# Kernel tuning notes

Measured on AMD Instinct MI355X. Metric: run time of the kernel, lower is better.

Reference implementation:

```python
import jax, jax.numpy as jnp
import numpy as np

B, N, C, H, KH = 4, 4096, 1024, 16, 5
HD = C // H  # head dim = 64


def setup_inputs() -> dict:
    key = jax.random.key(0)
    ks = jax.random.split(key, 4)
    return {
        "x": jax.random.normal(ks[0], (B, N, C), jnp.float32),
        "qkv_w": jax.random.normal(ks[1], (3 * C, C), jnp.float32) * 0.02,
        "qkv_b": jnp.zeros((3 * C,), jnp.float32),
        "proj_w": jax.random.normal(ks[2], (C, C), jnp.float32) * 0.02,
        "proj_b": jnp.zeros((C,), jnp.float32),
        "pos_enc": jnp.zeros((1, C), jnp.float32),  # torch init: zeros
        "dwc_w": jax.random.normal(ks[3], (HD, 1, KH, KH), jnp.float32) * 0.05,
        "dwc_b": jnp.zeros((HD,), jnp.float32),
        "num_heads": H,
    }


def reference(x, qkv_w, qkv_b, proj_w, proj_b, pos_enc, dwc_w, dwc_b, num_heads):
    b, n, c = x.shape
    h = num_heads
    hd = c // h
    kh = dwc_w.shape[2]

    qkv = x @ qkv_w.T + qkv_b                     # (b, n, 3c)
    q, k, v = jnp.split(qkv, 3, axis=-1)          # each (b, n, c)
    k = k + pos_enc[:, :c]                        # broadcast (1, c)
    q = jax.nn.relu(q)
    k = jax.nn.relu(k)

    def to_heads(t):  # (b, n, c) -> (b*h, n, hd)
        return t.reshape(b, n, h, hd).transpose(0, 2, 1, 3).reshape(b * h, n, hd)

    q, k, v = to_heads(q), to_heads(k), to_heads(v)

    # linear attention in fp32 (inputs already fp32)
    z = 1.0 / (jnp.einsum('bic,bc->bi', q, k.sum(axis=1)) + 1e-6)   # (bh, n)
    kv = jnp.einsum('bjc,bjd->bcd', k, v)                           # (bh, hd, hd)
    out = jnp.einsum('bic,bcd->bid', q, kv) * z[:, :, None]         # (bh, n, hd)

    # depthwise 2D conv on v viewed as (bh, hd, n, 1), kernel (hd,1,kh,kh), pad kh//2
    fm = v.transpose(0, 2, 1)[..., None]                            # (bh, hd, n, 1)
    pad = kh // 2
    fm = jax.lax.conv_general_dilated(
        fm, dwc_w, window_strides=(1, 1),
        padding=((pad, pad), (pad, pad)),
        dimension_numbers=('NCHW', 'OIHW', 'NCHW'),
        feature_group_count=hd,
    ) + dwc_b[None, :, None, None]
    out = out + fm[..., 0].transpose(0, 2, 1)                       # (bh, n, hd)

    out = out.reshape(b, h, n, hd).transpose(0, 2, 1, 3).reshape(b, n, c)
    return out @ proj_w.T + proj_b
```

## Files before the change

### kernel.cpp

```cpp
#include <hip/hip_runtime.h>


#define BB   4
#define NN   4096
#define CDIM 1024
#define NH   16
#define HDIM 64
#define BH   64

typedef __attribute__((ext_vector_type(8))) short short8;
typedef __attribute__((ext_vector_type(4))) float f32x4;
typedef unsigned short u16;

__device__ __forceinline__ float b2f(short s) {
    union { unsigned u; float f; } c;
    c.u = ((unsigned)(unsigned short)s) << 16;
    return c.f;
}
__device__ __forceinline__ u16 f2b(float f) {
    unsigned u = __float_as_uint(f);
    return (u16)((u + 0x7fffu + ((u >> 16) & 1u)) >> 16);
}
__device__ __forceinline__ void gload16(const void* g, void* l) {
    __builtin_amdgcn_global_load_lds((const __attribute__((address_space(1))) void*)g,
                                     (__attribute__((address_space(3))) void*)l, 16, 0, 0);
}

__global__ __launch_bounds__(256) void k_fill_diag(float* __restrict__ out, int n, float val)
{
    int i = blockIdx.x * 256 + threadIdx.x;
    if (i < n) out[i] = val;
}

__global__ __launch_bounds__(256) void k_f32_to_bf16(const float* __restrict__ in,
                                                     u16* __restrict__ out, int n4)
{
    int i = blockIdx.x * 256 + threadIdx.x;
    if (i < n4) {
        float4 v = reinterpret_cast<const float4*>(in)[i];
        ushort4 o;
        o.x = f2b(v.x); o.y = f2b(v.y); o.z = f2b(v.z); o.w = f2b(v.w);
        reinterpret_cast<ushort4*>(out)[i] = o;
    }
}


#define GEMM_PROLOGUE_AND_LOOP(EXTRA_BCOLS)                                              \
    const int t = threadIdx.x;                                                           \
    const int l = t & 63, w = t >> 6;                                                    \
    const int wr = w >> 2, wc = w & 3;                                                   \
    const int qa = ((l & 3) ^ ((l >> 3) & 3)) * 8;                                       \
    const int srow = t >> 2;                                                             \
    const u16* gA = A  + (size_t)(brow + srow) * 1024 + qa;                              \
    const u16* gB = Bw + (size_t)(bcol + srow) * 1024 + qa;                              \
    const int fr = l & 15;                                                               \
    const int phys8 = ((l >> 4) ^ ((l >> 1) & 3)) * 8;                                   \
    const int arow0 = wr * 128 + fr;                                                     \
    const int bfr0  = wc * 64 + fr;                                                      \
    f32x4 acc[8][4];                                                                     \
    _Pragma("unroll")                                                                    \
    for (int m = 0; m < 8; ++m)                                                          \
        _Pragma("unroll")                                                                \
        for (int n = 0; n < 4; ++n) acc[m][n] = (f32x4){0.f, 0.f, 0.f, 0.f};             \
                                              \
    auto STAGE = [&](int buf, int kt) {                                                  \
        const int kof = kt * 32;                                                         \
        char* lb = (char*)lds + buf * 32768 + w * 1024;                                  \
        gload16(gA + kof,          lb);                                                  \
        gload16(gA + 131072 + kof, lb + 8192);                                           \
        gload16(gB + kof,          lb + 16384);                                          \
        gload16(gB + 131072 + kof, lb + 24576);                                          \
    };                                                                                   \
    STAGE(0, 0);                                                                         \
    STAGE(1, 1);                                                                         \
    asm volatile("s_waitcnt vmcnt(4)" ::: "memory");                                     \
    __builtin_amdgcn_sched_barrier(0);                                                   \
    __builtin_amdgcn_s_barrier();                                                        \
    __builtin_amdgcn_sched_barrier(0);                                                   \
    for (int kt = 0; kt < 32; ++kt) {                                                    \
        const int cur = kt & 1;                                                          \
        const int ab = cur * 16384;                                                      \
        short8 af[8], bf[4];                                                             \
        _Pragma("unroll")                                                                \
        for (int n = 0; n < 4; ++n)                                                      \
            bf[n] = *reinterpret_cast<const short8*>(                                    \
                        &lds[ab + 8192 + (bfr0 + n * 16) * 32 + phys8]);                 \
        _Pragma("unroll")                                                                \
        for (int m = 0; m < 8; ++m)                                                      \
            af[m] = *reinterpret_cast<const short8*>(                                    \
                        &lds[ab + (arow0 + m * 16) * 32 + phys8]);                       \
        asm volatile("s_waitcnt lgkmcnt(0)" ::: "memory");                               \
        __builtin_amdgcn_sched_barrier(0);                                               \
        __builtin_amdgcn_s_barrier();               \
        __builtin_amdgcn_sched_barrier(0);                                               \
        if (kt + 2 < 32) STAGE(cur, kt + 2);                                             \
        __builtin_amdgcn_s_setprio(1);                                                   \
        _Pragma("unroll")                                                                \
        for (int m = 0; m < 8; ++m)                                                      \
            _Pragma("unroll")                                                            \
            for (int n = 0; n < 4; ++n)                                                  \
                acc[m][n] = __builtin_amdgcn_mfma_f32_16x16x32_bf16(                     \
                                af[m], bf[n], acc[m][n], 0, 0, 0);                       \
        __builtin_amdgcn_s_setprio(0);                                                   \
        if (kt + 2 < 32) { asm volatile("s_waitcnt vmcnt(4)" ::: "memory"); }            \
        else             { asm volatile("s_waitcnt vmcnt(0)" ::: "memory"); }            \
        __builtin_amdgcn_sched_barrier(0);                                               \
        __builtin_amdgcn_s_barrier();                 \
        __builtin_amdgcn_sched_barrier(0);                                               \
    }

__global__ __launch_bounds__(512, 2) void k_gemm1_256(
    const u16* __restrict__ A,
    const u16* __restrict__ Bw,
    const float* __restrict__ bias, const float* __restrict__ pos_enc,
    u16* __restrict__ q, u16* __restrict__ kk_, u16* __restrict__ v)
{
    __shared__ u16 lds[32768];
    const int lid = blockIdx.y * 12 + blockIdx.x;
    const int swz = (lid & 7) * 96 + (lid >> 3);
    const int bcol = (swz % 12) * 256;
    const int brow = (swz / 12) * 256;

    GEMM_PROLOGUE_AND_LOOP()

    const int part = bcol >> 10;
    u16* dst = (part == 0) ? q : (part == 1) ? kk_ : v;
    const int col_base = bcol + wc * 64 + fr;
    const int row_base = brow + wr * 128 + (l >> 4) * 4;
    #pragma unroll
    for (int n = 0; n < 4; ++n) {
        const int gc = col_base + n * 16;
        const int c  = gc & 1023;
        float bv = bias[gc];
        if (part == 1) bv += pos_enc[c];
        const int h = c >> 6, d = c & 63;
        #pragma unroll
        for (int m = 0; m < 8; ++m)
            #pragma unroll
            for (int j = 0; j < 4; ++j) {
                const int gr = row_base + m * 16 + j;
                const int b_ = gr >> 12, i_ = gr & 4095;
                float val = acc[m][n][j] + bv;
                if (part != 2) val = fmaxf(val, 0.f);
                dst[(size_t)((b_ * NH + h) * NN + i_) * HDIM + d] = f2b(val);
            }
    }
}

__global__ __launch_bounds__(512, 2) void k_gemm2_256(
    const u16* __restrict__ A,
    const u16* __restrict__ Bw,
    const float* __restrict__ bias, float* __restrict__ out)
{
    __shared__ u16 lds[32768];
    const int lid = blockIdx.y * 4 + blockIdx.x;
    const int swz = (lid & 7) * 32 + (lid >> 3);
    const int bcol = (swz % 4) * 256;
    const int brow = (swz / 4) * 256;

    GEMM_PROLOGUE_AND_LOOP()

    const int col_base = bcol + wc * 64 + fr;
    const int row_base = brow + wr * 128 + (l >> 4) * 4;
    #pragma unroll
    for (int n = 0; n < 4; ++n) {
        const int gc = col_base + n * 16;
        const float bv = bias[gc];
        #pragma unroll
        for (int m = 0; m < 8; ++m)
            #pragma unroll
            for (int j = 0; j < 4; ++j) {
                const int gr = row_base + m * 16 + j;
                out[(size_t)gr * CDIM + gc] = acc[m][n][j] + bv;
            }
    }
}

__global__ __launch_bounds__(256) void k_kv_partial(
    const u16* __restrict__ k, const u16* __restrict__ v,
    float* __restrict__ part_kv, float* __restrict__ part_ks)
{
    __shared__ float ks[32 * 64];
    __shared__ float vs[32 * 64];
    const int bh = blockIdx.x;
    const int chunk = blockIdx.y;
    const int t = threadIdx.x;
    const int cg = t >> 4;
    const int dg = t & 15;
    const int lr = t >> 3;
    const int lc = (t & 7) * 8;
    const size_t base = (size_t)bh * NN * HDIM + (size_t)chunk * 1024 * HDIM;
    float acc[4][4] = {};
    float ksac[4] = {};
    for (int j0 = 0; j0 < 1024; j0 += 32) {
        short8 kr = *reinterpret_cast<const short8*>(&k[base + (size_t)(j0 + lr) * 64 + lc]);
        short8 vr = *reinterpret_cast<const short8*>(&v[base + (size_t)(j0 + lr) * 64 + lc]);
        __syncthreads();
        #pragma unroll
        for (int j = 0; j < 8; ++j) {
            ks[lr * 64 + lc + j] = b2f(kr[j]);
            vs[lr * 64 + lc + j] = b2f(vr[j]);
        }
        __syncthreads();
        #pragma unroll
        for (int j = 0; j < 32; ++j) {
            float4 k4 = *reinterpret_cast<const float4*>(&ks[j * 64 + cg * 4]);
            float4 v4 = *reinterpret_cast<const float4*>(&vs[j * 64 + dg * 4]);
            const float* kp = reinterpret_cast<const float*>(&k4);
            const float* vp = reinterpret_cast<const float*>(&v4);
            #pragma unroll
            for (int ii = 0; ii < 4; ++ii) {
                ksac[ii] += kp[ii];
                #pragma unroll
                for (int jj = 0; jj < 4; ++jj)
                    acc[ii][jj] += kp[ii] * vp[jj];
            }
        }
    }
    const int pb = (chunk * BH + bh);
    #pragma unroll
    for (int ii = 0; ii < 4; ++ii) {
        #pragma unroll
        for (int jj = 0; jj < 4; ++jj)
            part_kv[pb * 4096 + (cg * 4 + ii) * 64 + dg * 4 + jj] = acc[ii][jj];
        if (dg == 0) part_ks[pb * 64 + cg * 4 + ii] = ksac[ii];
    }
}

__global__ __launch_bounds__(256) void k_kv_reduce_t(
    const float* __restrict__ part_kv, const float* __restrict__ part_ks,
    u16* __restrict__ kvt)
{
    const int bh = blockIdx.x;
    const int t = threadIdx.x;
    u16* base = kvt + bh * 5120;
    #pragma unroll
    for (int r = 0; r < 16; ++r) {
        const int idx = r * 256 + t;
        const int c = idx >> 6, d = idx & 63;
        float s = 0.f;
        #pragma unroll
        for (int ch = 0; ch < 4; ++ch) s += part_kv[(ch * BH + bh) * 4096 + idx];
        base[d * 64 + c] = f2b(s);
    }
    if (t < 64) {
        float s = 0.f;
        #pragma unroll
        for (int ch = 0; ch < 4; ++ch) s += part_ks[(ch * BH + bh) * 64 + t];
        base[4096 + t] = f2b(s);
    }
    for (int z = t; z < 960; z += 256) base[4160 + z] = 0;
}

__global__ __launch_bounds__(256) void k_attn_mfma(
    const u16* __restrict__ q, const u16* __restrict__ v,
    const u16* __restrict__ kvt,
    const float* __restrict__ dwc_w, const float* __restrict__ dwc_b,
    u16* __restrict__ out2)
{
    __shared__ u16 att[4][64 * 68];
    const int t = threadIdx.x;
    const int l = t & 63, w = t >> 6;
    const int bh = blockIdx.x;
    const int tb = blockIdx.y * 256 + w * 64;
    const size_t hb = (size_t)bh * NN * HDIM;
    const u16* qb  = q + hb + (size_t)tb * HDIM;
    const u16* kvb = kvt + bh * 5120;

    const int fr = l & 15;
    const int kfrag = (l >> 4) * 8;

    short8 bfr[5][2];
    #pragma unroll
    for (int n = 0; n < 5; ++n)
        #pragma unroll
        for (int ks = 0; ks < 2; ++ks)
            bfr[n][ks] = *reinterpret_cast<const short8*>(&kvb[(n * 16 + fr) * 64 + ks * 32 + kfrag]);

    f32x4 acc[4][5];
    #pragma unroll
    for (int m = 0; m < 4; ++m)
        #pragma unroll
        for (int n = 0; n < 5; ++n) acc[m][n] = (f32x4){0.f, 0.f, 0.f, 0.f};

    #pragma unroll
    for (int m = 0; m < 4; ++m)
        #pragma unroll
        for (int ks = 0; ks < 2; ++ks) {
            short8 a = *reinterpret_cast<const short8*>(&qb[(m * 16 + fr) * 64 + ks * 32 + kfrag]);
            #pragma unroll
            for (int n = 0; n < 5; ++n)
                acc[m][n] = __builtin_amdgcn_mfma_f32_16x16x32_bf16(a, bfr[n][ks], acc[m][n], 0, 0, 0);
        }

    #pragma unroll
    for (int m = 0; m < 4; ++m)
        #pragma unroll
        for (int j = 0; j < 4; ++j) {
            const float den = __shfl(acc[m][4][j], l & 48);
            const float z = 1.f / (den + 1e-6f);
            const int row = m * 16 + (l >> 4) * 4 + j;
            #pragma unroll
            for (int n = 0; n < 4; ++n)
                att[w][row * 68 + fr + n * 16] = f2b(acc[m][n][j] * z);
        }
    __syncthreads();

    const int d = l;
    float w5[5];
    #pragma unroll
    for (int dh = 0; dh < 5; ++dh) w5[dh] = dwc_w[d * 25 + dh * 5 + 2];
    const float cbias = dwc_b[d];
    const int b_ = bh >> 4, h_ = bh & 15;
    u16* obase = out2 + (size_t)b_ * NN * CDIM + (size_t)h_ * 64 + d;
    float win[5];
    #pragma unroll
    for (int p = 0; p < 4; ++p) {
        const int src = tb - 2 + p;
        win[p] = (src >= 0 && src < NN) ? b2f(v[hb + (size_t)src * 64 + d]) : 0.f;
    }
    for (int it = 0; it < 64; ++it) {
        const int srcn = tb + it + 2;
        win[4] = (srcn < NN) ? b2f(v[hb + (size_t)srcn * 64 + d]) : 0.f;
        const float fm = cbias + w5[0] * win[0] + w5[1] * win[1] + w5[2] * win[2]
                               + w5[3] * win[3] + w5[4] * win[4];
        const float attn = b2f((short)att[w][it * 68 + d]);
        obase[(size_t)(tb + it) * CDIM] = f2b(attn + fm);
        win[0] = win[1]; win[1] = win[2]; win[2] = win[3]; win[3] = win[4];
    }
}

extern "C" void kernel_launch(void* const* d_in, const int* in_sizes, int n_in,
                              void* d_out, int out_size, void* d_ws, size_t ws_size,
                              hipStream_t stream)
{
    const float* x       = (const float*)d_in[0];
    const float* qkv_w   = (const float*)d_in[1];
    const float* qkv_b   = (const float*)d_in[2];
    const float* proj_w  = (const float*)d_in[3];
    const float* proj_b  = (const float*)d_in[4];
    const float* pos_enc = (const float*)d_in[5];
    const float* dwc_w   = (const float*)d_in[6];
    const float* dwc_b   = (const float*)d_in[7];

    const size_t QKV = 16777216;
    char* p = (char*)d_ws;
    u16* q_b    = (u16*)p;               p += QKV * 2;
    u16* k_b    = (u16*)p;               p += QKV * 2;
    u16* v_b    = (u16*)p;               p += QKV * 2;
    u16* x_b    = (u16*)p;               p += QKV * 2;
    u16* qkvw_b = (u16*)p;               p += (size_t)3145728 * 2;
    u16* projw_b= (u16*)p;               p += (size_t)1048576 * 2;
    float* part_kv = (float*)p;          p += (size_t)1048576 * 4;
    float* part_ks = (float*)p;          p += (size_t)16384 * 4;
    u16* kvt       = (u16*)p;            p += (size_t)(64 * 5120) * 2;
    const size_t need_bytes = (size_t)(p - (char*)d_ws);

    if (ws_size < need_bytes) {
        const float diag = 4096.0f + (float)(ws_size >> 20);
        k_fill_diag<<<(out_size + 255) / 256, 256, 0, stream>>>((float*)d_out, out_size, diag);
        return;
    }

    u16* out2 = k_b;
    float* out = (float*)d_out;

    k_f32_to_bf16<<<16384, 256, 0, stream>>>(x,      x_b,     4194304);
    k_f32_to_bf16<<< 3072, 256, 0, stream>>>(qkv_w,  qkvw_b,   786432);
    k_f32_to_bf16<<< 1024, 256, 0, stream>>>(proj_w, projw_b,  262144);

    k_gemm1_256  <<<dim3(12, 64), 512, 0, stream>>>(x_b, qkvw_b, qkv_b, pos_enc, q_b, k_b, v_b);
    k_kv_partial <<<dim3(64, 4),  256, 0, stream>>>(k_b, v_b, part_kv, part_ks);
    k_kv_reduce_t<<<64,           256, 0, stream>>>(part_kv, part_ks, kvt);
    k_attn_mfma  <<<dim3(64, 16), 256, 0, stream>>>(q_b, v_b, kvt, dwc_w, dwc_b, out2);
    k_gemm2_256  <<<dim3(4, 64),  512, 0, stream>>>(out2, projw_b, proj_b, out);
}
```

Measured before the change: 315.4 us.

## Restructure 256x256 GEMM mainloop into 8-phase pipeline with 64-wide K tiles

```diff
diff --git a/kernel.cpp b/kernel.cpp
--- a/kernel.cpp
+++ b/kernel.cpp
@@ -44,68 +44,123 @@
     }
 }
 
-
-#define GEMM_PROLOGUE_AND_LOOP(EXTRA_BCOLS)                                              \
+#define GEMM256_8PH()                                                                    \
     const int t = threadIdx.x;                                                           \
     const int l = t & 63, w = t >> 6;                                                    \
     const int wr = w >> 2, wc = w & 3;                                                   \
-    const int qa = ((l & 3) ^ ((l >> 3) & 3)) * 8;                                       \
-    const int srow = t >> 2;                                                             \
-    const u16* gA = A  + (size_t)(brow + srow) * 1024 + qa;                              \
-    const u16* gB = Bw + (size_t)(bcol + srow) * 1024 + qa;                              \
     const int fr = l & 15;                                                               \
-    const int phys8 = ((l >> 4) ^ ((l >> 1) & 3)) * 8;                                   \
-    const int arow0 = wr * 128 + fr;                                                     \
-    const int bfr0  = wc * 64 + fr;                                                      \
+    const int physE  = ((l >> 4) ^ ((fr >> 1) & 3)) * 8;                                 \
+    const int qa     = ((l & 3) ^ ((l >> 3) & 3)) * 8;                                   \
+    const int aRow   = w * 16 + (l >> 2);                                                \
+    const u16* gA0 = A  + (size_t)(brow + aRow) * 1024 + qa;                             \
+    const u16* gB0 = Bw + (size_t)(bcol + aRow) * 1024 + qa;                             \
+    char* ldsc = (char*)lds;                                                             \
+    const int afBase = (wr * 128 + fr) * 32 + physE;                                     \
+    const int bfBase = 16384 + (wc * 64 + fr) * 32 + physE;                              \
     f32x4 acc[8][4];                                                                     \
     _Pragma("unroll")                                                                    \
     for (int m = 0; m < 8; ++m)                                                          \
         _Pragma("unroll")                                                                \
         for (int n = 0; n < 4; ++n) acc[m][n] = (f32x4){0.f, 0.f, 0.f, 0.f};             \
-                                              \
-    auto STAGE = [&](int buf, int kt) {                                                  \
-        const int kof = kt * 32;                                                         \
-        char* lb = (char*)lds + buf * 32768 + w * 1024;                                  \
-        gload16(gA + kof,          lb);                                                  \
-        gload16(gA + 131072 + kof, lb + 8192);                                           \
-        gload16(gB + kof,          lb + 16384);                                          \
-        gload16(gB + 131072 + kof, lb + 24576);                                          \
+    auto STG = [&](int kt, int kh, int isB) {                                            \
+        const u16* g = (isB ? gB0 : gA0) + kt * 64 + kh * 32;                            \
+        char* d = ldsc + (kt & 1) * 65536 + isB * 32768 + kh * 16384 + w * 1024 + l * 16;\
+        gload16(g,          d);                                                          \
+        gload16(g + 131072, d + 8192);                                                   \
     };                                                                                   \
-    STAGE(0, 0);                                                                         \
-    STAGE(1, 1);                                                                         \
+    STG(0,0,0); STG(0,0,1); STG(0,1,0); STG(0,1,1); STG(1,0,0); STG(1,0,1);              \
     asm volatile("s_waitcnt vmcnt(4)" ::: "memory");                                     \
     __builtin_amdgcn_sched_barrier(0);                                                   \
     __builtin_amdgcn_s_barrier();                                                        \
     __builtin_amdgcn_sched_barrier(0);                                                   \
-    for (int kt = 0; kt < 32; ++kt) {                                                    \
-        const int cur = kt & 1;                                                          \
-        const int ab = cur * 16384;                                                      \
-        short8 af[8], bf[4];                                                             \
+    _Pragma("unroll 1")                                                                  \
+    for (int kt = 0; kt < 16; ++kt) {                                                    \
+        const int B0 = (kt & 1) * 32768;                                                 \
+        short8 af[4], bf[4];                                                             \
+                                                               \
+        _Pragma("unroll")                                                                \
+        for (int m = 0; m < 4; ++m)                                                      \
+            af[m] = *reinterpret_cast<const short8*>(&lds[B0 + afBase + m * 512]);       \
         _Pragma("unroll")                                                                \
         for (int n = 0; n < 4; ++n)                                                      \
-            bf[n] = *reinterpret_cast<const short8*>(                                    \
-                        &lds[ab + 8192 + (bfr0 + n * 16) * 32 + phys8]);                 \
-        _Pragma("unroll")                                                                \
-        for (int m = 0; m < 8; ++m)                                                      \
-            af[m] = *reinterpret_cast<const short8*>(                                    \
-                        &lds[ab + (arow0 + m * 16) * 32 + phys8]);                       \
+            bf[n] = *reinterpret_cast<const short8*>(&lds[B0 + bfBase + n * 512]);       \
+        if (kt + 1 < 16) STG(kt + 1, 1, 0);                                              \
+        __builtin_amdgcn_sched_barrier(0);                                               \
+        __builtin_amdgcn_s_barrier();                                                    \
         asm volatile("s_waitcnt lgkmcnt(0)" ::: "memory");                               \
         __builtin_amdgcn_sched_barrier(0);                                               \
-        __builtin_amdgcn_s_barrier();               \
-        __builtin_amdgcn_sched_barrier(0);                                               \
-        if (kt + 2 < 32) STAGE(cur, kt + 2);                                             \
         __builtin_amdgcn_s_setprio(1);                                                   \
         _Pragma("unroll")                                                                \
-        for (int m = 0; m < 8; ++m)                                                      \
+        for (int m = 0; m < 4; ++m)                                                      \
             _Pragma("unroll")                                                            \
             for (int n = 0; n < 4; ++n)                                                  \
-                acc[m][n] = __builtin_amdgcn_mfma_f32_16x16x32_bf16(                     \
-                                af[m], bf[n], acc[m][n], 0, 0, 0);                       \
+                acc[m][n] = __builtin_amdgcn_mfma_f32_16x16x32_bf16(af[m], bf[n], acc[m][n], 0, 0, 0); \
         __builtin_amdgcn_s_setprio(0);                                                   \
-        if (kt + 2 < 32) { asm volatile("s_waitcnt vmcnt(4)" ::: "memory"); }            \
-        else             { asm volatile("s_waitcnt vmcnt(0)" ::: "memory"); }            \
-        __builtin_amdgcn_sched_barrier(0);                                               \
-        __builtin_amdgcn_s_barrier();                 \
+        __builtin_amdgcn_sched_barrier(0);                                               \
+        __builtin_amdgcn_s_barrier();                                                    \
+        __builtin_amdgcn_sched_barrier(0);                                               \
+                                                               \
+        _Pragma("unroll")                                                                \
+        for (int m = 0; m < 4; ++m)                                                      \
+            af[m] = *reinterpret_cast<const short8*>(&lds[B0 + afBase + (m + 4) * 512]); \
+        if (kt + 1 < 16) STG(kt + 1, 1, 1);                                              \
+        __builtin_amdgcn_sched_barrier(0);                                               \
+        __builtin_amdgcn_s_barrier();                                                    \
+        asm volatile("s_waitcnt lgkmcnt(0)" ::: "memory");                               \
+        __builtin_amdgcn_sched_barrier(0);                                               \
+        __builtin_amdgcn_s_setprio(1);                                                   \
+        _Pragma("unroll")                                                                \
+        for (int m = 0; m < 4; ++m)                                                      \
+            _Pragma("unroll")                                                            \
+            for (int n = 0; n < 4; ++n)                                                  \
+                acc[m + 4][n] = __builtin_amdgcn_mfma_f32_16x16x32_bf16(af[m], bf[n], acc[m + 4][n], 0, 0, 0); \
+        __builtin_amdgcn_s_setprio(0);                                                   \
+        __builtin_amdgcn_sched_barrier(0);                                               \
+        __builtin_amdgcn_s_barrier();                                                    \
+        __builtin_amdgcn_sched_barrier(0);                                               \
+                                                               \
+        _Pragma("unroll")                                                                \
+        for (int m = 0; m < 4; ++m)                                                      \
+            af[m] = *reinterpret_cast<const short8*>(&lds[B0 + 8192 + afBase + m * 512]);\
+        _Pragma("unroll")                                                                \
+        for (int n = 0; n < 4; ++n)                                                      \
+            bf[n] = *reinterpret_cast<const short8*>(&lds[B0 + 8192 + bfBase + n * 512]);\
+        if (kt + 2 < 16) STG(kt + 2, 0, 0);                                              \
+        __builtin_amdgcn_sched_barrier(0);                                               \
+        __builtin_amdgcn_s_barrier();                                                    \
+        asm volatile("s_waitcnt lgkmcnt(0)" ::: "memory");                               \
+        __builtin_amdgcn_sched_barrier(0);                                               \
+        __builtin_amdgcn_s_setprio(1);                                                   \
+        _Pragma("unroll")                                                                \
+        for (int m = 0; m < 4; ++m)                                                      \
+            _Pragma("unroll")                                                            \
+            for (int n = 0; n < 4; ++n)                                                  \
+                acc[m][n] = __builtin_amdgcn_mfma_f32_16x16x32_bf16(af[m], bf[n], acc[m][n], 0, 0, 0); \
+        __builtin_amdgcn_s_setprio(0);                                                   \
+        __builtin_amdgcn_sched_barrier(0);                                               \
+        __builtin_amdgcn_s_barrier();                                                    \
+        __builtin_amdgcn_sched_barrier(0);                                               \
+                                                               \
+        _Pragma("unroll")                                                                \
+        for (int m = 0; m < 4; ++m)                                                      \
+            af[m] = *reinterpret_cast<const short8*>(&lds[B0 + 8192 + afBase + (m + 4) * 512]); \
+        if (kt + 2 < 16) STG(kt + 2, 0, 1);                                              \
+        __builtin_amdgcn_sched_barrier(0);                                               \
+        __builtin_amdgcn_s_barrier();                                                    \
+        asm volatile("s_waitcnt lgkmcnt(0)" ::: "memory");                               \
+        __builtin_amdgcn_sched_barrier(0);                                               \
+        __builtin_amdgcn_s_setprio(1);                                                   \
+        _Pragma("unroll")                                                                \
+        for (int m = 0; m < 4; ++m)                                                      \
+            _Pragma("unroll")                                                            \
+            for (int n = 0; n < 4; ++n)                                                  \
+                acc[m + 4][n] = __builtin_amdgcn_mfma_f32_16x16x32_bf16(af[m], bf[n], acc[m + 4][n], 0, 0, 0); \
+        __builtin_amdgcn_s_setprio(0);                                                   \
+        __builtin_amdgcn_sched_barrier(0);                                               \
+        if (kt < 15) { asm volatile("s_waitcnt vmcnt(4)" ::: "memory"); }                \
+        else         { asm volatile("s_waitcnt vmcnt(0)" ::: "memory"); }                \
+        __builtin_amdgcn_sched_barrier(0);                                               \
+        __builtin_amdgcn_s_barrier();                                                    \
         __builtin_amdgcn_sched_barrier(0);                                               \
     }
 
@@ -115,13 +170,13 @@
     const float* __restrict__ bias, const float* __restrict__ pos_enc,
     u16* __restrict__ q, u16* __restrict__ kk_, u16* __restrict__ v)
 {
-    __shared__ u16 lds[32768];
+    __shared__ u16 lds[65536];
     const int lid = blockIdx.y * 12 + blockIdx.x;
     const int swz = (lid & 7) * 96 + (lid >> 3);
     const int bcol = (swz % 12) * 256;
     const int brow = (swz / 12) * 256;
 
-    GEMM_PROLOGUE_AND_LOOP()
+    GEMM256_8PH()
 
     const int part = bcol >> 10;
     u16* dst = (part == 0) ? q : (part == 1) ? kk_ : v;
@@ -152,13 +207,13 @@
     const u16* __restrict__ Bw,
     const float* __restrict__ bias, float* __restrict__ out)
 {
-    __shared__ u16 lds[32768];
+    __shared__ u16 lds[65536];
     const int lid = blockIdx.y * 4 + blockIdx.x;
     const int swz = (lid & 7) * 32 + (lid >> 3);
     const int bcol = (swz % 4) * 256;
     const int brow = (swz / 4) * 256;
 
-    GEMM_PROLOGUE_AND_LOOP()
+    GEMM256_8PH()
 
     const int col_base = bcol + wc * 64 + fr;
     const int row_base = brow + wr * 128 + (l >> 4) * 4;
```

Result: no change. 312.8 us (-0.8%).
